# Performance work log

Hardware: AMD Instinct MI355X
Metric: run time of the kernel (lower is better)

## Reference

```python
import jax, jax.numpy as jnp
import numpy as np

EPS = 1e-06
H, D_MODEL = 16, 1024
DK = D_MODEL // H
B, S = 16, 4096


def elu_fea_map(x):
    return jax.nn.elu(x) + 1.0


def setup_inputs() -> dict:
    key = jax.random.key(0)
    ks = jax.random.split(key, 11)
    lim = 1.0 / np.sqrt(D_MODEL)
    u = lambda k, shp: jax.random.uniform(k, shp, jnp.float32, -lim, lim)
    return {
        "query": jax.random.normal(ks[0], (B, D_MODEL), jnp.float32),
        "key": jax.random.normal(ks[1], (B, S, D_MODEL), jnp.float32),
        "value": jax.random.normal(ks[2], (B, S, D_MODEL), jnp.float32),
        "Wq": u(ks[3], (D_MODEL, D_MODEL)), "bq": u(ks[4], (D_MODEL,)),
        "Wk": u(ks[5], (D_MODEL, D_MODEL)), "bk": u(ks[6], (D_MODEL,)),
        "Wv": u(ks[7], (D_MODEL, D_MODEL)), "bv": u(ks[8], (D_MODEL,)),
        "Wo": u(ks[9], (D_MODEL, D_MODEL)), "bo": u(ks[10], (D_MODEL,)),
    }


def reference(query, key, value, Wq, bq, Wk, bk, Wv, bv, Wo, bo):
    nb = query.shape[0]
    # projections; torch Linear: x @ W.T + b
    q = (query @ Wq.T + bq).reshape(nb, 1, H, DK)   # [B,1,H,D]
    k = (key @ Wk.T + bk).reshape(nb, -1, H, DK)    # [B,S,H,D]
    v = (value @ Wv.T + bv).reshape(nb, -1, H, DK)  # [B,S,H,M]
    Q = elu_fea_map(q)
    K = elu_fea_map(k)
    KV = jnp.einsum('bshd,bshm->bhdm', K, v)                      # [B,H,D,M]
    Z = 1.0 / (jnp.einsum('bshd,bhd->bsh', Q, K.sum(axis=1)) + EPS)  # [B,1,H]
    V = jnp.einsum('bshd,bhdm,bsh->bshm', Q, KV, Z)               # [B,1,H,M]
    x = V.reshape(nb, H * DK)
    return x @ Wo.T + bo
```

## Files before the change

### kernel.cpp

```cpp
#include <hip/hip_runtime.h>
#include <hip/hip_bf16.h>
#include <stdint.h>


using bf16 = __hip_bfloat16;
typedef __attribute__((ext_vector_type(8))) short short8;
typedef __attribute__((ext_vector_type(4))) float f32x4;

#define NB_B 16
#define SEQ 4096
#define DM 1024
#define NH 16
#define DKH 64

__device__ __forceinline__ void gload_lds16(const void* g, void* l) {
  __builtin_amdgcn_global_load_lds((const __attribute__((address_space(1))) void*)g,
                                   (__attribute__((address_space(3))) void*)l, 16, 0, 0);
}

__device__ __forceinline__ short8 cvt8(f32x4 a, f32x4 b) {
  union { bf16 h[8]; short8 v; } pk;
  pk.h[0] = __float2bfloat16(a[0]); pk.h[1] = __float2bfloat16(a[1]);
  pk.h[2] = __float2bfloat16(a[2]); pk.h[3] = __float2bfloat16(a[3]);
  pk.h[4] = __float2bfloat16(b[0]); pk.h[5] = __float2bfloat16(b[1]);
  pk.h[6] = __float2bfloat16(b[2]); pk.h[7] = __float2bfloat16(b[3]);
  return pk.v;
}

__global__ __launch_bounds__(256) void conv_kernel(const float* __restrict__ src,
                                                   bf16* __restrict__ dst, long n4) {
  long i = (long)blockIdx.x * blockDim.x + threadIdx.x;
  const long stride = (long)gridDim.x * blockDim.x;
  for (; i < n4; i += stride) {
    float4 v = ((const float4*)src)[i];
    union { ushort4 u; bf16 h[4]; } o;
    o.h[0] = __float2bfloat16(v.x);
    o.h[1] = __float2bfloat16(v.y);
    o.h[2] = __float2bfloat16(v.z);
    o.h[3] = __float2bfloat16(v.w);
    ((ushort4*)dst)[i] = o.u;
  }
}

template <int KPROJ>
__global__ __launch_bounds__(512, 2) void gemm256(
    const float* __restrict__ A, const bf16* __restrict__ W,
    const float* __restrict__ bias, bf16* __restrict__ outT,
    float* __restrict__ Ksum, int rowsTot, int b0, int chunk) {
  __shared__ float As[3][256 * 32];
  __shared__ bf16 Bs[3][256 * 32];
  const int tid = threadIdx.x;
  const int lane = tid & 63;
  const int wid = tid >> 6;
  const int wr = wid >> 2;
  const int wc = wid & 3;
  const int wgid = (blockIdx.x & 7) * chunk + (blockIdx.x >> 3);
  const int row0 = (wgid >> 2) * 256;
  const int col0 = (wgid & 3) * 256;

  f32x4 acc[8][4] = {};

  const int lr = lane & 15;
  const int xrA = (lr & 7) << 4;
  const int xrB = ((lr >> 1) & 3) << 4;
  const int ksA = (lane >> 4) * 32;
  const int ksB = (lane >> 4) * 16;

  const float* Ag = A + (long)(row0 + wid * 8 + (lane >> 3)) * DM +
                    (((lane & 7) ^ (lane >> 3)) << 2);
  const bf16* Wg = W + (long)(col0 + wid * 16 + (lane >> 2)) * DM +
                   (((lane & 3) ^ ((lane >> 3) & 3)) << 3);

#define ISSUE_AB(ib, kt_) { \
  _Pragma("unroll") for (int j = 0; j < 4; ++j) \
    gload_lds16(Ag + (long)(j * 64) * DM + (kt_) * 32, \
                (void*)((char*)As[ib] + (wid * 8 + j * 64) * 128)); \
  _Pragma("unroll") for (int j = 0; j < 2; ++j) \
    gload_lds16(Wg + (long)(j * 128) * DM + (kt_) * 32, \
                (void*)((char*)Bs[ib] + (wid * 16 + j * 128) * 64)); }

#define TILE_BODY(buf) { \
  const char* AscB = (const char*)As[buf]; \
  const char* BscB = (const char*)Bs[buf]; \
  short8 af[4], bfv[4]; \
  _Pragma("unroll") for (int m = 0; m < 4; ++m) { \
    const int rb = (wr * 128 + m * 16 + lr) * 128; \
    f32x4 a0 = *(const f32x4*)(AscB + rb + (ksA ^ xrA)); \
    f32x4 a1 = *(const f32x4*)(AscB + rb + ((ksA + 16) ^ xrA)); \
    af[m] = cvt8(a0, a1); } \
  _Pragma("unroll") for (int n = 0; n < 4; ++n) \
    bfv[n] = *(const short8*)(BscB + (wc * 64 + n * 16 + lr) * 64 + (ksB ^ xrB)); \
  __builtin_amdgcn_sched_barrier(0); \
  __builtin_amdgcn_s_setprio(1); \
  _Pragma("unroll") for (int m = 0; m < 4; ++m) \
    _Pragma("unroll") for (int n = 0; n < 4; ++n) \
      acc[m][n] = __builtin_amdgcn_mfma_f32_16x16x32_bf16(af[m], bfv[n], acc[m][n], 0, 0, 0); \
  __builtin_amdgcn_s_setprio(0); \
  asm volatile("s_barrier" ::: "memory"); \
  _Pragma("unroll") for (int m = 0; m < 4; ++m) { \
    const int rb = (wr * 128 + (m + 4) * 16 + lr) * 128; \
    f32x4 a0 = *(const f32x4*)(AscB + rb + (ksA ^ xrA)); \
    f32x4 a1 = *(const f32x4*)(AscB + rb + ((ksA + 16) ^ xrA)); \
    af[m] = cvt8(a0, a1); } \
  asm volatile("s_barrier" ::: "memory"); \
  __builtin_amdgcn_sched_barrier(0); \
  __builtin_amdgcn_s_setprio(1); \
  _Pragma("unroll") for (int m = 0; m < 4; ++m) \
    _Pragma("unroll") for (int n = 0; n < 4; ++n) \
      acc[m + 4][n] = __builtin_amdgcn_mfma_f32_16x16x32_bf16(af[m], bfv[n], acc[m + 4][n], 0, 0, 0); \
  __builtin_amdgcn_s_setprio(0); \
  asm volatile("s_barrier" ::: "memory"); }

  ISSUE_AB(0, 0)
  ISSUE_AB(1, 1)

#pragma unroll 1
  for (int kt3 = 0; kt3 < 30; kt3 += 3) {
    ISSUE_AB(2, kt3 + 2)
    asm volatile("s_waitcnt vmcnt(12)\n\ts_barrier" ::: "memory");
    TILE_BODY(0)
    ISSUE_AB(0, kt3 + 3)
    asm volatile("s_waitcnt vmcnt(12)\n\ts_barrier" ::: "memory");
    TILE_BODY(1)
    ISSUE_AB(1, kt3 + 4)
    asm volatile("s_waitcnt vmcnt(12)\n\ts_barrier" ::: "memory");
    TILE_BODY(2)
  }
  asm volatile("s_waitcnt vmcnt(6)\n\ts_barrier" ::: "memory");
  TILE_BODY(0)
  asm volatile("s_waitcnt vmcnt(0)\n\ts_barrier" ::: "memory");
  TILE_BODY(1)

#undef ISSUE_AB
#undef TILE_BODY

  const int bglob = b0 + (row0 >> 12);
#pragma unroll
  for (int n = 0; n < 4; ++n) {
    const int colg = col0 + wc * 64 + n * 16 + lr;
    const float bv = bias[colg];
    float csum = 0.f;
#pragma unroll
    for (int m = 0; m < 8; ++m) {
      const int r = row0 + wr * 128 + m * 16 + (lane >> 4) * 4;
      union { ushort4 u; bf16 h[4]; } pk;
#pragma unroll
      for (int i = 0; i < 4; ++i) {
        float v = acc[m][n][i] + bv;
        if (KPROJ) { v = v > 0.f ? v + 1.f : __expf(v); csum += v; }
        pk.h[i] = __float2bfloat16(v);
      }
      *(ushort4*)&outT[(long)colg * rowsTot + r] = pk.u;
    }
    if (KPROJ) {
      csum += __shfl_xor(csum, 16);
      csum += __shfl_xor(csum, 32);
      if (lane < 16) atomicAdd(&Ksum[(long)bglob * DM + colg], csum);
    }
  }
}

__global__ __launch_bounds__(256) void kv_kernel(
    const bf16* __restrict__ KT, const bf16* __restrict__ VT,
    float* __restrict__ KVp, int rowsTot, int b0) {
  const int sp = blockIdx.x & 3;
  const int h = (blockIdx.x >> 2) & 15;
  const int b_loc = blockIdx.x >> 6;
  const int lane = threadIdx.x & 63;
  const int w = threadIdx.x >> 6;
  const long srow = (long)b_loc * SEQ + sp * (SEQ / 4) + ((lane >> 4) * 8);
  const bf16* Ab = KT + (long)(h * DKH + w * 16 + (lane & 15)) * rowsTot + srow;
  const bf16* Bb = VT + (long)(h * DKH + (lane & 15)) * rowsTot + srow;
  f32x4 acc[4] = {};
#pragma unroll 4
  for (int s = 0; s < SEQ / 4; s += 32) {
    short8 a = *(const short8*)(Ab + s);
#pragma unroll
    for (int n = 0; n < 4; ++n) {
      short8 bv = *(const short8*)(Bb + (long)n * 16 * rowsTot + s);
      acc[n] = __builtin_amdgcn_mfma_f32_16x16x32_bf16(a, bv, acc[n], 0, 0, 0);
    }
  }
  float* o = KVp + (((long)sp * NB_B + (b0 + b_loc)) * NH + h) * DKH * DKH;
#pragma unroll
  for (int n = 0; n < 4; ++n)
#pragma unroll
    for (int i = 0; i < 4; ++i)
      o[(w * 16 + (lane >> 4) * 4 + i) * DKH + n * 16 + (lane & 15)] = acc[n][i];
}

template <int ELU>
__global__ __launch_bounds__(256) void vecmat_kernel(
    const float* __restrict__ in, const float* __restrict__ W,
    const float* __restrict__ bias, float* __restrict__ outp) {
  const int b = blockIdx.x >> 5;
  const int n0 = (blockIdx.x & 31) * 32;
  const int lane = threadIdx.x & 63;
  const int w = threadIdx.x >> 6;
  float4 qv[4];
#pragma unroll
  for (int it = 0; it < 4; ++it)
    qv[it] = *(const float4*)&in[(long)b * DM + it * 256 + lane * 4];
#pragma unroll
  for (int j = 0; j < 8; ++j) {
    const int n = n0 + w * 8 + j;
    const float* wrow = W + (long)n * DM;
    float s = 0.f;
#pragma unroll
    for (int it = 0; it < 4; ++it) {
      float4 wv = *(const float4*)&wrow[it * 256 + lane * 4];
      s += qv[it].x * wv.x + qv[it].y * wv.y + qv[it].z * wv.z + qv[it].w * wv.w;
    }
    s += __shfl_xor(s, 1);  s += __shfl_xor(s, 2);  s += __shfl_xor(s, 4);
    s += __shfl_xor(s, 8);  s += __shfl_xor(s, 16); s += __shfl_xor(s, 32);
    if (lane == 0) {
      float v = s + bias[n];
      if (ELU) v = v > 0.f ? v + 1.f : __expf(v);
      outp[(long)b * DM + n] = v;
    }
  }
}

__global__ __launch_bounds__(256) void xcomp_kernel(
    const float* __restrict__ Q, const float* __restrict__ KVp,
    const float* __restrict__ Ksum, float* __restrict__ xb) {
  const int b = blockIdx.x;
  const int t = threadIdx.x;
  const int h = t >> 4;
  const int m0 = (t & 15) * 4;
  const float* q = Q + (long)b * DM + h * DKH;
  const float* ks = Ksum + (long)b * DM + h * DKH;
  const long kvoff = ((long)b * NH + h) * DKH * DKH;
  const long spstride = (long)NB_B * NH * DKH * DKH;
  float zden = 0.f;
#pragma unroll
  for (int d = 0; d < DKH; ++d) zden += q[d] * ks[d];
  const float z = 1.f / (zden + 1e-6f);
  float nv[4] = {0.f, 0.f, 0.f, 0.f};
  for (int d = 0; d < DKH; ++d) {
    const float qd = q[d];
#pragma unroll
    for (int j = 0; j < 4; ++j) {
      const long idx = kvoff + d * DKH + m0 + j;
      nv[j] += qd * (KVp[idx] + KVp[idx + spstride] +
                     KVp[idx + 2 * spstride] + KVp[idx + 3 * spstride]);
    }
  }
  float* xo = xb + (long)b * DM + h * DKH + m0;
#pragma unroll
  for (int j = 0; j < 4; ++j) xo[j] = nv[j] * z;
}

extern "C" void kernel_launch(void* const* d_in, const int* in_sizes, int n_in,
                              void* d_out, int out_size, void* d_ws, size_t ws_size,
                              hipStream_t stream) {
  (void)in_sizes; (void)n_in; (void)out_size;
  const float* query = (const float*)d_in[0];
  const float* key   = (const float*)d_in[1];
  const float* value = (const float*)d_in[2];
  const float* Wq = (const float*)d_in[3];
  const float* bq = (const float*)d_in[4];
  const float* Wk = (const float*)d_in[5];
  const float* bk = (const float*)d_in[6];
  const float* Wv = (const float*)d_in[7];
  const float* bv = (const float*)d_in[8];
  const float* Wo = (const float*)d_in[9];
  const float* bo = (const float*)d_in[10];
  float* out = (float*)d_out;

  char* p = (char*)d_ws;
  bf16* WkB = (bf16*)p;  p += (size_t)DM * DM * 2;
  bf16* WvB = (bf16*)p;  p += (size_t)DM * DM * 2;
  float* KVp = (float*)p; p += (size_t)4 * NB_B * NH * DKH * DKH * 4;
  float* Ksum = (float*)p; p += (size_t)NB_B * DM * 4;
  float* Q = (float*)p;  p += (size_t)NB_B * DM * 4;
  float* xb = (float*)p; p += (size_t)NB_B * DM * 4;
  const size_t fixed = (size_t)(p - (char*)d_ws);
  const size_t per_b = (size_t)2 * SEQ * DM * 2;
  if (ws_size < fixed + per_b) return;
  int nbc = (int)((ws_size - fixed) / per_b);
  if (nbc > NB_B) nbc = NB_B;
  bf16* kT = (bf16*)p; p += (size_t)nbc * SEQ * DM * 2;
  bf16* vT = (bf16*)p; p += (size_t)nbc * SEQ * DM * 2;

  hipMemsetAsync(Ksum, 0, (size_t)NB_B * DM * 4, stream);
  conv_kernel<<<512, 256, 0, stream>>>(Wk, WkB, (long)DM * DM / 4);
  conv_kernel<<<512, 256, 0, stream>>>(Wv, WvB, (long)DM * DM / 4);
  vecmat_kernel<1><<<NB_B * 32, 256, 0, stream>>>(query, Wq, bq, Q);

  for (int b0 = 0; b0 < NB_B; b0 += nbc) {
    const int nb = (NB_B - b0 < nbc) ? (NB_B - b0) : nbc;
    const int rows = nb * SEQ;
    const int nwg = (rows / 256) * 4;
    gemm256<1><<<nwg, 512, 0, stream>>>(key + (size_t)b0 * SEQ * DM, WkB, bk, kT, Ksum, rows, b0, nwg / 8);
    gemm256<0><<<nwg, 512, 0, stream>>>(value + (size_t)b0 * SEQ * DM, WvB, bv, vT, (float*)nullptr, rows, b0, nwg / 8);
    kv_kernel<<<nb * NH * 4, 256, 0, stream>>>(kT, vT, KVp, rows, b0);
  }

  xcomp_kernel<<<NB_B, 256, 0, stream>>>(Q, KVp, Ksum, xb);
  vecmat_kernel<0><<<NB_B * 32, 256, 0, stream>>>(xb, Wo, bo, out);
}
```

Before: 693.8 us.

## Restructure GEMM pipeline with 64-wide B tiles and interleaved half-step loads

Changes the projection GEMM's B (weight) staging from three 32-wide K buffers to two 64-wide K buffers, and splits each step so A and B global-to-LDS loads are issued at different points inside the compute step. Barriers per step drop from four to two, and waitcnt values are tuned per half. The goal is to reduce synchronization overhead and overlap memory traffic with MFMA work better. This adds risk of race conditions in buffer reuse and changes the LDS footprint and swizzle pattern.

```diff
diff --git a/kernel.cpp b/kernel.cpp
--- a/kernel.cpp
+++ b/kernel.cpp
@@ -48,7 +48,7 @@
     const float* __restrict__ bias, bf16* __restrict__ outT,
     float* __restrict__ Ksum, int rowsTot, int b0, int chunk) {
   __shared__ float As[3][256 * 32];
-  __shared__ bf16 Bs[3][256 * 32];
+  __shared__ bf16 Bs[2][256 * 64];
   const int tid = threadIdx.x;
   const int lane = tid & 63;
   const int wid = tid >> 6;
@@ -61,78 +61,91 @@
   f32x4 acc[8][4] = {};
 
   const int lr = lane & 15;
-  const int xrA = (lr & 7) << 4;
-  const int xrB = ((lr >> 1) & 3) << 4;
-  const int ksA = (lane >> 4) * 32;
-  const int ksB = (lane >> 4) * 16;
+  const int xr = (lr & 7) << 4;
+  const int g32 = (lane >> 4) * 32;
+  const int g16 = (lane >> 4) * 16;
 
   const float* Ag = A + (long)(row0 + wid * 8 + (lane >> 3)) * DM +
                     (((lane & 7) ^ (lane >> 3)) << 2);
-  const bf16* Wg = W + (long)(col0 + wid * 16 + (lane >> 2)) * DM +
-                   (((lane & 3) ^ ((lane >> 3) & 3)) << 3);
-
-#define ISSUE_AB(ib, kt_) { \
-  _Pragma("unroll") for (int j = 0; j < 4; ++j) \
-    gload_lds16(Ag + (long)(j * 64) * DM + (kt_) * 32, \
-                (void*)((char*)As[ib] + (wid * 8 + j * 64) * 128)); \
-  _Pragma("unroll") for (int j = 0; j < 2; ++j) \
-    gload_lds16(Wg + (long)(j * 128) * DM + (kt_) * 32, \
-                (void*)((char*)Bs[ib] + (wid * 16 + j * 128) * 64)); }
-
-#define TILE_BODY(buf) { \
-  const char* AscB = (const char*)As[buf]; \
-  const char* BscB = (const char*)Bs[buf]; \
-  short8 af[4], bfv[4]; \
-  _Pragma("unroll") for (int m = 0; m < 4; ++m) { \
-    const int rb = (wr * 128 + m * 16 + lr) * 128; \
-    f32x4 a0 = *(const f32x4*)(AscB + rb + (ksA ^ xrA)); \
-    f32x4 a1 = *(const f32x4*)(AscB + rb + ((ksA + 16) ^ xrA)); \
-    af[m] = cvt8(a0, a1); } \
-  _Pragma("unroll") for (int n = 0; n < 4; ++n) \
-    bfv[n] = *(const short8*)(BscB + (wc * 64 + n * 16 + lr) * 64 + (ksB ^ xrB)); \
-  __builtin_amdgcn_sched_barrier(0); \
-  __builtin_amdgcn_s_setprio(1); \
-  _Pragma("unroll") for (int m = 0; m < 4; ++m) \
+  const bf16* Wg = W + (long)(col0 + wid * 8 + (lane >> 3)) * DM +
+                   (((lane & 7) ^ (lane >> 3)) << 3);
+
+#define SA_ONE(dstbuf, j, H_) \
+  gload_lds16(Ag + (long)((j) * 64) * DM + (H_) * 32, \
+              (void*)&As[dstbuf][(wid * 8 + (j) * 64) * 32]);
+#define SB_ONE(dstbuf, j, T_) \
+  gload_lds16(Wg + (long)((j) * 64) * DM + (T_) * 64, \
+              (void*)&Bs[dstbuf][(wid * 8 + (j) * 64) * 64]);
+
+#define STEP(H, AB, BB, HALF, SA, SB, VMS) { \
+    asm volatile("s_waitcnt vmcnt(" VMS ")\n\ts_barrier" ::: "memory"); \
+    if (SB) { SB_ONE((BB) ^ 1, 2 * (HALF), ((H) >> 1) + 1) \
+              SB_ONE((BB) ^ 1, 2 * (HALF) + 1, ((H) >> 1) + 1) } \
+    const char* AsB = (const char*)As[(AB)]; \
+    const char* BsB = (const char*)Bs[(BB)]; \
+    short8 af[4], bfv[4]; \
+    _Pragma("unroll") for (int m = 0; m < 4; ++m) { \
+      const int rb = (wr * 128 + m * 16 + lr) * 128; \
+      f32x4 a0 = *(const f32x4*)(AsB + rb + (g32 ^ xr)); \
+      f32x4 a1 = *(const f32x4*)(AsB + rb + ((g32 + 16) ^ xr)); \
+      af[m] = cvt8(a0, a1); } \
     _Pragma("unroll") for (int n = 0; n < 4; ++n) \
-      acc[m][n] = __builtin_amdgcn_mfma_f32_16x16x32_bf16(af[m], bfv[n], acc[m][n], 0, 0, 0); \
-  __builtin_amdgcn_s_setprio(0); \
-  asm volatile("s_barrier" ::: "memory"); \
-  _Pragma("unroll") for (int m = 0; m < 4; ++m) { \
-    const int rb = (wr * 128 + (m + 4) * 16 + lr) * 128; \
-    f32x4 a0 = *(const f32x4*)(AscB + rb + (ksA ^ xrA)); \
-    f32x4 a1 = *(const f32x4*)(AscB + rb + ((ksA + 16) ^ xrA)); \
-    af[m] = cvt8(a0, a1); } \
-  asm volatile("s_barrier" ::: "memory"); \
-  __builtin_amdgcn_sched_barrier(0); \
-  __builtin_amdgcn_s_setprio(1); \
-  _Pragma("unroll") for (int m = 0; m < 4; ++m) \
-    _Pragma("unroll") for (int n = 0; n < 4; ++n) \
-      acc[m + 4][n] = __builtin_amdgcn_mfma_f32_16x16x32_bf16(af[m], bfv[n], acc[m + 4][n], 0, 0, 0); \
-  __builtin_amdgcn_s_setprio(0); \
-  asm volatile("s_barrier" ::: "memory"); }
-
-  ISSUE_AB(0, 0)
-  ISSUE_AB(1, 1)
+      bfv[n] = *(const short8*)(BsB + (wc * 64 + n * 16 + lr) * 128 + \
+                                (((HALF) * 64 + g16) ^ xr)); \
+    __builtin_amdgcn_s_setprio(1); \
+    _Pragma("unroll") for (int m = 0; m < 4; ++m) \
+      _Pragma("unroll") for (int n = 0; n < 4; ++n) \
+        acc[m][n] = __builtin_amdgcn_mfma_f32_16x16x32_bf16(af[m], bfv[n], acc[m][n], 0, 0, 0); \
+    __builtin_amdgcn_s_setprio(0); \
+    asm volatile("s_barrier" ::: "memory"); \
+    if (SA) { _Pragma("unroll") for (int j = 0; j < 4; ++j) \
+                SA_ONE(((AB) + 2) % 3, j, (H) + 2) } \
+    _Pragma("unroll") for (int m = 0; m < 4; ++m) { \
+      const int rb = (wr * 128 + (m + 4) * 16 + lr) * 128; \
+      f32x4 a0 = *(const f32x4*)(AsB + rb + (g32 ^ xr)); \
+      f32x4 a1 = *(const f32x4*)(AsB + rb + ((g32 + 16) ^ xr)); \
+      af[m] = cvt8(a0, a1); } \
+    __builtin_amdgcn_s_setprio(1); \
+    _Pragma("unroll") for (int m = 0; m < 4; ++m) \
+      _Pragma("unroll") for (int n = 0; n < 4; ++n) \
+        acc[m + 4][n] = __builtin_amdgcn_mfma_f32_16x16x32_bf16(af[m], bfv[n], acc[m + 4][n], 0, 0, 0); \
+    __builtin_amdgcn_s_setprio(0); \
+  }
+
+  SB_ONE(0, 0, 0) SB_ONE(0, 1, 0)
+#pragma unroll
+  for (int j = 0; j < 4; ++j) SA_ONE(0, j, 0)
+  SB_ONE(0, 2, 0) SB_ONE(0, 3, 0)
+#pragma unroll
+  for (int j = 0; j < 4; ++j) SA_ONE(1, j, 1)
 
 #pragma unroll 1
-  for (int kt3 = 0; kt3 < 30; kt3 += 3) {
-    ISSUE_AB(2, kt3 + 2)
-    asm volatile("s_waitcnt vmcnt(12)\n\ts_barrier" ::: "memory");
-    TILE_BODY(0)
-    ISSUE_AB(0, kt3 + 3)
-    asm volatile("s_waitcnt vmcnt(12)\n\ts_barrier" ::: "memory");
-    TILE_BODY(1)
-    ISSUE_AB(1, kt3 + 4)
-    asm volatile("s_waitcnt vmcnt(12)\n\ts_barrier" ::: "memory");
-    TILE_BODY(2)
-  }
-  asm volatile("s_waitcnt vmcnt(6)\n\ts_barrier" ::: "memory");
-  TILE_BODY(0)
-  asm volatile("s_waitcnt vmcnt(0)\n\ts_barrier" ::: "memory");
-  TILE_BODY(1)
-
-#undef ISSUE_AB
-#undef TILE_BODY
+  for (int hb = 0; hb < 24; hb += 12) {
+    STEP(hb + 0, 0, 0, 0, 1, 1, "4")
+    STEP(hb + 1, 1, 0, 1, 1, 1, "6")
+    STEP(hb + 2, 2, 1, 0, 1, 1, "4")
+    STEP(hb + 3, 0, 1, 1, 1, 1, "6")
+    STEP(hb + 4, 1, 0, 0, 1, 1, "4")
+    STEP(hb + 5, 2, 0, 1, 1, 1, "6")
+    STEP(hb + 6, 0, 1, 0, 1, 1, "4")
+    STEP(hb + 7, 1, 1, 1, 1, 1, "6")
+    STEP(hb + 8, 2, 0, 0, 1, 1, "4")
+    STEP(hb + 9, 0, 0, 1, 1, 1, "6")
+    STEP(hb + 10, 1, 1, 0, 1, 1, "4")
+    STEP(hb + 11, 2, 1, 1, 1, 1, "6")
+  }
+  STEP(24, 0, 0, 0, 1, 1, "4")
+  STEP(25, 1, 0, 1, 1, 1, "6")
+  STEP(26, 2, 1, 0, 1, 1, "4")
+  STEP(27, 0, 1, 1, 1, 1, "6")
+  STEP(28, 1, 0, 0, 1, 1, "4")
+  STEP(29, 2, 0, 1, 1, 1, "6")
+  STEP(30, 0, 1, 0, 0, 0, "4")
+  STEP(31, 1, 1, 1, 0, 0, "0")
+
+#undef STEP
+#undef SA_ONE
+#undef SB_ONE
 
   const int bglob = b0 + (row0 >> 12);
 #pragma unroll
```

Result: faster. 642.4 us (-7.4%).

## Stage fp32 A through registers into bf16 LDS with 64-wide K tiles

Applied to the files above, without the earlier changes.

The projection GEMM main loop is restructured. The fp32 A operand is now loaded from global memory into registers, converted to bf16 once, and written to a double-buffered bf16 LDS tile, instead of being copied fp32 straight into LDS and converted on every fragment read. The K tile grows from 32 to 64, halving the iteration count and cutting barriers per K element, while W keeps a triple-buffered direct-to-LDS path. This should lower LDS footprint and bandwidth and remove redundant conversions, at the cost of more registers for the staged A data and a more complex wait/barrier schedule.

```diff
diff --git a/kernel.cpp b/kernel.cpp
--- a/kernel.cpp
+++ b/kernel.cpp
@@ -18,12 +18,12 @@
                                    (__attribute__((address_space(3))) void*)l, 16, 0, 0);
 }
 
-__device__ __forceinline__ short8 cvt8(f32x4 a, f32x4 b) {
+__device__ __forceinline__ short8 cvt8(float4 a, float4 b) {
   union { bf16 h[8]; short8 v; } pk;
-  pk.h[0] = __float2bfloat16(a[0]); pk.h[1] = __float2bfloat16(a[1]);
-  pk.h[2] = __float2bfloat16(a[2]); pk.h[3] = __float2bfloat16(a[3]);
-  pk.h[4] = __float2bfloat16(b[0]); pk.h[5] = __float2bfloat16(b[1]);
-  pk.h[6] = __float2bfloat16(b[2]); pk.h[7] = __float2bfloat16(b[3]);
+  pk.h[0] = __float2bfloat16(a.x); pk.h[1] = __float2bfloat16(a.y);
+  pk.h[2] = __float2bfloat16(a.z); pk.h[3] = __float2bfloat16(a.w);
+  pk.h[4] = __float2bfloat16(b.x); pk.h[5] = __float2bfloat16(b.y);
+  pk.h[6] = __float2bfloat16(b.z); pk.h[7] = __float2bfloat16(b.w);
   return pk.v;
 }
 
@@ -47,8 +47,8 @@
     const float* __restrict__ A, const bf16* __restrict__ W,
     const float* __restrict__ bias, bf16* __restrict__ outT,
     float* __restrict__ Ksum, int rowsTot, int b0, int chunk) {
-  __shared__ float As[3][256 * 32];
-  __shared__ bf16 Bs[3][256 * 32];
+  __shared__ bf16 As[2][256 * 64];
+  __shared__ bf16 Bs[3][256 * 64];
   const int tid = threadIdx.x;
   const int lane = tid & 63;
   const int wid = tid >> 6;
@@ -61,78 +61,103 @@
   f32x4 acc[8][4] = {};
 
   const int lr = lane & 15;
-  const int xrA = (lr & 7) << 4;
-  const int xrB = ((lr >> 1) & 3) << 4;
-  const int ksA = (lane >> 4) * 32;
-  const int ksB = (lane >> 4) * 16;
-
-  const float* Ag = A + (long)(row0 + wid * 8 + (lane >> 3)) * DM +
-                    (((lane & 7) ^ (lane >> 3)) << 2);
-  const bf16* Wg = W + (long)(col0 + wid * 16 + (lane >> 2)) * DM +
-                   (((lane & 3) ^ ((lane >> 3) & 3)) << 3);
-
-#define ISSUE_AB(ib, kt_) { \
+  const int xr = (lane & 7) << 4;
+  const int lk = (lane >> 4) * 16;
+
+  const float* Afp = A + (long)(row0 + wid * 32 + (lane >> 3)) * DM + (lane & 7) * 8;
+  const int awbyte = (wid * 32 + (lane >> 3)) * 128 + (((lane & 7) ^ (lane >> 3)) << 4);
+  const bf16* Wg = W + (long)(col0 + wid * 32 + (lane >> 3)) * DM +
+                   ((lane & 7) ^ (lane >> 3)) * 8;
+  const int sdstB = wid * 32 * 64;
+
+  float4 fa[8];
+
+#define SB_STAGE(buf, T_) { \
   _Pragma("unroll") for (int j = 0; j < 4; ++j) \
-    gload_lds16(Ag + (long)(j * 64) * DM + (kt_) * 32, \
-                (void*)((char*)As[ib] + (wid * 8 + j * 64) * 128)); \
-  _Pragma("unroll") for (int j = 0; j < 2; ++j) \
-    gload_lds16(Wg + (long)(j * 128) * DM + (kt_) * 32, \
-                (void*)((char*)Bs[ib] + (wid * 16 + j * 128) * 64)); }
-
-#define TILE_BODY(buf) { \
-  const char* AscB = (const char*)As[buf]; \
-  const char* BscB = (const char*)Bs[buf]; \
-  short8 af[4], bfv[4]; \
-  _Pragma("unroll") for (int m = 0; m < 4; ++m) { \
-    const int rb = (wr * 128 + m * 16 + lr) * 128; \
-    f32x4 a0 = *(const f32x4*)(AscB + rb + (ksA ^ xrA)); \
-    f32x4 a1 = *(const f32x4*)(AscB + rb + ((ksA + 16) ^ xrA)); \
-    af[m] = cvt8(a0, a1); } \
-  _Pragma("unroll") for (int n = 0; n < 4; ++n) \
-    bfv[n] = *(const short8*)(BscB + (wc * 64 + n * 16 + lr) * 64 + (ksB ^ xrB)); \
-  __builtin_amdgcn_sched_barrier(0); \
-  __builtin_amdgcn_s_setprio(1); \
-  _Pragma("unroll") for (int m = 0; m < 4; ++m) \
+    gload_lds16(Wg + (long)j * 8 * DM + (T_) * 64, (void*)&Bs[buf][sdstB + j * 512]); }
+
+#define A_ISSUE(T_) { \
+  _Pragma("unroll") for (int j = 0; j < 4; ++j) { \
+    fa[2 * j]     = *(const float4*)(Afp + (long)j * 8 * DM + (T_) * 64); \
+    fa[2 * j + 1] = *(const float4*)(Afp + (long)j * 8 * DM + (T_) * 64 + 4); } }
+
+#define A_WRITE(NAB) { \
+  _Pragma("unroll") for (int j = 0; j < 4; ++j) \
+    *(short8*)((char*)As[NAB] + awbyte + j * 1024) = cvt8(fa[2 * j], fa[2 * j + 1]); }
+
+#define TILE(t_, AB, BB, NAB, NBB, SA, SB) { \
+    if (SA) A_ISSUE((t_) + 1)                       \
+    if (SB) SB_STAGE(NBB, (t_) + 2)                 \
+    const char* AsB = (const char*)As[AB]; \
+    const char* BsB = (const char*)Bs[BB]; \
+    short8 af[4], bfv[4]; \
+     \
+    _Pragma("unroll") for (int m = 0; m < 4; ++m) \
+      af[m] = *(const short8*)(AsB + (wr * 128 + m * 16 + lr) * 128 + (lk ^ xr)); \
     _Pragma("unroll") for (int n = 0; n < 4; ++n) \
-      acc[m][n] = __builtin_amdgcn_mfma_f32_16x16x32_bf16(af[m], bfv[n], acc[m][n], 0, 0, 0); \
-  __builtin_amdgcn_s_setprio(0); \
-  asm volatile("s_barrier" ::: "memory"); \
-  _Pragma("unroll") for (int m = 0; m < 4; ++m) { \
-    const int rb = (wr * 128 + (m + 4) * 16 + lr) * 128; \
-    f32x4 a0 = *(const f32x4*)(AscB + rb + (ksA ^ xrA)); \
-    f32x4 a1 = *(const f32x4*)(AscB + rb + ((ksA + 16) ^ xrA)); \
-    af[m] = cvt8(a0, a1); } \
-  asm volatile("s_barrier" ::: "memory"); \
-  __builtin_amdgcn_sched_barrier(0); \
-  __builtin_amdgcn_s_setprio(1); \
-  _Pragma("unroll") for (int m = 0; m < 4; ++m) \
+      bfv[n] = *(const short8*)(BsB + (wc * 64 + n * 16 + lr) * 128 + (lk ^ xr)); \
+    __builtin_amdgcn_s_setprio(1); \
+    _Pragma("unroll") for (int m = 0; m < 4; ++m) \
+      _Pragma("unroll") for (int n = 0; n < 4; ++n) \
+        acc[m][n] = __builtin_amdgcn_mfma_f32_16x16x32_bf16(af[m], bfv[n], acc[m][n], 0, 0, 0); \
+    __builtin_amdgcn_s_setprio(0); \
+    asm volatile("s_barrier" ::: "memory"); \
+     \
+    _Pragma("unroll") for (int m = 0; m < 4; ++m) \
+      af[m] = *(const short8*)(AsB + (wr * 128 + (m + 4) * 16 + lr) * 128 + (lk ^ xr)); \
+    __builtin_amdgcn_s_setprio(1); \
+    _Pragma("unroll") for (int m = 0; m < 4; ++m) \
+      _Pragma("unroll") for (int n = 0; n < 4; ++n) \
+        acc[m + 4][n] = __builtin_amdgcn_mfma_f32_16x16x32_bf16(af[m], bfv[n], acc[m + 4][n], 0, 0, 0); \
+    __builtin_amdgcn_s_setprio(0); \
+    asm volatile("s_barrier" ::: "memory"); \
+     \
+    _Pragma("unroll") for (int m = 0; m < 4; ++m) \
+      af[m] = *(const short8*)(AsB + (wr * 128 + m * 16 + lr) * 128 + ((64 + lk) ^ xr)); \
     _Pragma("unroll") for (int n = 0; n < 4; ++n) \
-      acc[m + 4][n] = __builtin_amdgcn_mfma_f32_16x16x32_bf16(af[m], bfv[n], acc[m + 4][n], 0, 0, 0); \
-  __builtin_amdgcn_s_setprio(0); \
-  asm volatile("s_barrier" ::: "memory"); }
-
-  ISSUE_AB(0, 0)
-  ISSUE_AB(1, 1)
+      bfv[n] = *(const short8*)(BsB + (wc * 64 + n * 16 + lr) * 128 + ((64 + lk) ^ xr)); \
+    __builtin_amdgcn_s_setprio(1); \
+    _Pragma("unroll") for (int m = 0; m < 4; ++m) \
+      _Pragma("unroll") for (int n = 0; n < 4; ++n) \
+        acc[m][n] = __builtin_amdgcn_mfma_f32_16x16x32_bf16(af[m], bfv[n], acc[m][n], 0, 0, 0); \
+    __builtin_amdgcn_s_setprio(0); \
+    asm volatile("s_barrier" ::: "memory"); \
+     \
+    if (SA) A_WRITE(NAB)                   \
+    _Pragma("unroll") for (int m = 0; m < 4; ++m) \
+      af[m] = *(const short8*)(AsB + (wr * 128 + (m + 4) * 16 + lr) * 128 + ((64 + lk) ^ xr)); \
+    __builtin_amdgcn_s_setprio(1); \
+    _Pragma("unroll") for (int m = 0; m < 4; ++m) \
+      _Pragma("unroll") for (int n = 0; n < 4; ++n) \
+        acc[m + 4][n] = __builtin_amdgcn_mfma_f32_16x16x32_bf16(af[m], bfv[n], acc[m + 4][n], 0, 0, 0); \
+    __builtin_amdgcn_s_setprio(0); \
+    asm volatile("s_waitcnt lgkmcnt(0)\n\ts_barrier" ::: "memory"); \
+  }
+
+  A_ISSUE(0)
+  SB_STAGE(0, 0)
+  SB_STAGE(1, 1)
+  A_WRITE(0)
+  asm volatile("s_waitcnt vmcnt(4) lgkmcnt(0)\n\ts_barrier" ::: "memory");
 
 #pragma unroll 1
-  for (int kt3 = 0; kt3 < 30; kt3 += 3) {
-    ISSUE_AB(2, kt3 + 2)
-    asm volatile("s_waitcnt vmcnt(12)\n\ts_barrier" ::: "memory");
-    TILE_BODY(0)
-    ISSUE_AB(0, kt3 + 3)
-    asm volatile("s_waitcnt vmcnt(12)\n\ts_barrier" ::: "memory");
-    TILE_BODY(1)
-    ISSUE_AB(1, kt3 + 4)
-    asm volatile("s_waitcnt vmcnt(12)\n\ts_barrier" ::: "memory");
-    TILE_BODY(2)
-  }
-  asm volatile("s_waitcnt vmcnt(6)\n\ts_barrier" ::: "memory");
-  TILE_BODY(0)
-  asm volatile("s_waitcnt vmcnt(0)\n\ts_barrier" ::: "memory");
-  TILE_BODY(1)
-
-#undef ISSUE_AB
-#undef TILE_BODY
+  for (int tb = 0; tb < 12; tb += 6) {
+    TILE(tb + 0, 0, 0, 1, 2, 1, 1)
+    TILE(tb + 1, 1, 1, 0, 0, 1, 1)
+    TILE(tb + 2, 0, 2, 1, 1, 1, 1)
+    TILE(tb + 3, 1, 0, 0, 2, 1, 1)
+    TILE(tb + 4, 0, 1, 1, 0, 1, 1)
+    TILE(tb + 5, 1, 2, 0, 1, 1, 1)
+  }
+  TILE(12, 0, 0, 1, 2, 1, 1)
+  TILE(13, 1, 1, 0, 0, 1, 1)
+  TILE(14, 0, 2, 1, 1, 1, 0)
+  TILE(15, 1, 0, 0, 0, 0, 0)
+
+#undef TILE
+#undef A_ISSUE
+#undef A_WRITE
+#undef SB_STAGE
 
   const int bglob = b0 + (row0 >> 12);
 #pragma unroll
```

After: 660.5 us. 4.8% less time.
